# Optimization experiments

Measured on AMD Instinct MI355X. Metric: run time of the kernel, lower is better.

## Reference

```python
import jax, jax.numpy as jnp
import numpy as np

N = 50000
E = 800000
IN_F = 128
HID = 128
OUT_F = 64
MU = 2.0
EPS = 1e-12


def setup_inputs() -> dict:
    key = jax.random.key(0)
    ks = jax.random.split(key, 20)
    d = {}
    d["x"] = jax.random.normal(ks[0], (N, IN_F), dtype=jnp.float32)
    d["edge_src"] = jax.random.randint(ks[1], (E,), 0, N, dtype=jnp.int32)
    d["edge_dst"] = jax.random.randint(ks[2], (E,), 0, N, dtype=jnp.int32)
    d["edge_val"] = jax.random.uniform(ks[3], (E,), dtype=jnp.float32)
    # layer 0: in=128 -> pool=128 -> out=128 (activation=relu)
    s0 = 1.0 / np.sqrt(IN_F)
    d["pool_w0"] = jax.random.uniform(ks[4], (IN_F, IN_F), jnp.float32, -s0, s0)
    d["pool_b0"] = jax.random.uniform(ks[5], (IN_F,), jnp.float32, -s0, s0)
    d["fc1_w0"] = jax.random.uniform(ks[6], (HID, IN_F), jnp.float32, -s0, s0)
    d["fc1_b0"] = jax.random.uniform(ks[7], (HID,), jnp.float32, -s0, s0)
    d["fc2_w0"] = jax.random.uniform(ks[8], (HID, IN_F), jnp.float32, -s0, s0)
    d["fc2_b0"] = jax.random.uniform(ks[9], (HID,), jnp.float32, -s0, s0)
    # layer 1 (final): in=128 -> pool=128 -> out=64 (no activation)
    s1 = 1.0 / np.sqrt(HID)
    d["pool_w1"] = jax.random.uniform(ks[10], (HID, HID), jnp.float32, -s1, s1)
    d["pool_b1"] = jax.random.uniform(ks[11], (HID,), jnp.float32, -s1, s1)
    d["fc1_w1"] = jax.random.uniform(ks[12], (OUT_F, HID), jnp.float32, -s1, s1)
    d["fc1_b1"] = jax.random.uniform(ks[13], (OUT_F,), jnp.float32, -s1, s1)
    d["fc2_w1"] = jax.random.uniform(ks[14], (OUT_F, HID), jnp.float32, -s1, s1)
    d["fc2_b1"] = jax.random.uniform(ks[15], (OUT_F,), jnp.float32, -s1, s1)
    return d


def _sage_conv(x, src, dst, val, pw, pb, w1, b1, w2, b2, act):
    # L2-normalize rows (F.normalize(x, dim=1))
    xn = x / jnp.maximum(jnp.linalg.norm(x, axis=1, keepdims=True), EPS)
    h = jax.nn.relu(xn @ pw.T + pb)               # [N, pool]
    h_mu = h ** MU                                # elementwise pow
    # spmm(adj, h_mu): gather source rows, scale by edge weight, scatter-add to dst rows
    agg = jax.ops.segment_sum(h_mu[src] * val[:, None], dst, num_segments=N)
    agg = agg ** (1.0 / MU)                       # generalized-mean root
    out = (h @ w1.T + b1) + (agg @ w2.T + b2)
    return jax.nn.relu(out) if act else out


def reference(x, edge_src, edge_dst, edge_val,
              pool_w0, pool_b0, fc1_w0, fc1_b0, fc2_w0, fc2_b0,
              pool_w1, pool_b1, fc1_w1, fc1_b1, fc2_w1, fc2_b1):
    h = _sage_conv(x, edge_src, edge_dst, edge_val,
                   pool_w0, pool_b0, fc1_w0, fc1_b0, fc2_w0, fc2_b0, act=True)
    out = _sage_conv(h, edge_src, edge_dst, edge_val,
                     pool_w1, pool_b1, fc1_w1, fc1_b1, fc2_w1, fc2_b1, act=False)
    return out
```

## Files before the change

### kernel.cpp

```cpp
#include <hip/hip_runtime.h>

#define FF 128
#define BCAP 8192
#define CHUNK 4096

typedef __attribute__((ext_vector_type(8))) short short8;
typedef __attribute__((ext_vector_type(4))) float f32x4;

__device__ __forceinline__ unsigned short bf16_rne(float f) {
    unsigned u = __float_as_uint(f);
    u += 0x7fffu + ((u >> 16) & 1u);
    return (unsigned short)(u >> 16);
}
__device__ __forceinline__ float bf16_to_f32(unsigned short h) {
    return __uint_as_float(((unsigned)h) << 16);
}

template<int ABF16>
__global__ __launch_bounds__(256, 2)
void pool_mfma(const void* __restrict__ xin_,
               const unsigned short* __restrict__ Wh, const unsigned short* __restrict__ Wl,
               const float* __restrict__ bias,
               unsigned short* __restrict__ hout, unsigned short* __restrict__ hsqout, int N)
{
    constexpr int PITCH = 136;
    __shared__ unsigned short sX[64 * PITCH];
    __shared__ float sNorm[64];

    const int tid  = threadIdx.x;
    const int tile = blockIdx.x;

    #pragma unroll
    for (int rg = 0; rg < 2; ++rg) {
        const int row = rg * 32 + (tid >> 3);
        const int c0  = (tid & 7) * 16;
        const int n   = tile * 64 + row;
        const int base = row * PITCH + c0;
        float ss = 0.f;
        if constexpr (ABF16) {
            const unsigned short* xin = (const unsigned short*)xin_;
            union { short8 s; unsigned short u[8]; } a, b;
            short8 z = {0,0,0,0,0,0,0,0};
            a.s = z; b.s = z;
            if (n < N) {
                const short8* p = (const short8*)(xin + (size_t)n * FF + c0);
                a.s = p[0]; b.s = p[1];
            }
            #pragma unroll
            for (int i = 0; i < 8; ++i) {
                float fa = bf16_to_f32(a.u[i]);
                float fb = bf16_to_f32(b.u[i]);
                ss = fmaf(fa, fa, fmaf(fb, fb, ss));
            }
            *(short8*)&sX[base]     = a.s;
            *(short8*)&sX[base + 8] = b.s;
        } else {
            const float* xin = (const float*)xin_;
            float v[16];
            if (n < N) {
                const float4* p = (const float4*)(xin + (size_t)n * FF + c0);
                #pragma unroll
                for (int i = 0; i < 4; ++i) {
                    float4 q = p[i];
                    v[4*i] = q.x; v[4*i+1] = q.y; v[4*i+2] = q.z; v[4*i+3] = q.w;
                }
            } else {
                #pragma unroll
                for (int i = 0; i < 16; ++i) v[i] = 0.f;
            }
            #pragma unroll
            for (int i = 0; i < 16; ++i) ss = fmaf(v[i], v[i], ss);
            union { unsigned short u[8]; short8 s; } h0, h1;
            #pragma unroll
            for (int i = 0; i < 8; ++i) {
                h0.u[i] = bf16_rne(v[i]);
                h1.u[i] = bf16_rne(v[8 + i]);
            }
            *(short8*)&sX[base]     = h0.s;
            *(short8*)&sX[base + 8] = h1.s;
        }
        ss += __shfl_xor(ss, 1);
        ss += __shfl_xor(ss, 2);
        ss += __shfl_xor(ss, 4);
        if ((tid & 7) == 0) sNorm[row] = 1.0f / fmaxf(sqrtf(ss), 1e-12f);
    }
    __syncthreads();

    const int lane = tid & 63, wave = tid >> 6;
    const int quad = lane >> 4, l16 = lane & 15;

    short8 Bh[2][4], Bl[2][4];
    #pragma unroll
    for (int c = 0; c < 2; ++c) {
        const int jt = 2 * wave + c;
        #pragma unroll
        for (int t = 0; t < 4; ++t) {
            const size_t o = ((size_t)(jt * 4 + t) * 64 + lane) * 8;
            Bh[c][t] = *(const short8*)&Wh[o];
            Bl[c][t] = *(const short8*)&Wl[o];
        }
    }

    f32x4 acc[4][2];
    #pragma unroll
    for (int r = 0; r < 4; ++r)
        #pragma unroll
        for (int c = 0; c < 2; ++c) {
            f32x4 z = {0.f, 0.f, 0.f, 0.f};
            acc[r][c] = z;
        }

    #pragma unroll
    for (int t = 0; t < 4; ++t) {
        short8 Ah[4];
        #pragma unroll
        for (int r = 0; r < 4; ++r)
            Ah[r] = *(const short8*)&sX[(r * 16 + l16) * PITCH + t * 32 + quad * 8];
        #pragma unroll
        for (int c = 0; c < 2; ++c)
            #pragma unroll
            for (int r = 0; r < 4; ++r) {
                acc[r][c] = __builtin_amdgcn_mfma_f32_16x16x32_bf16(Ah[r], Bh[c][t], acc[r][c], 0, 0, 0);
                acc[r][c] = __builtin_amdgcn_mfma_f32_16x16x32_bf16(Ah[r], Bl[c][t], acc[r][c], 0, 0, 0);
            }
    }

    #pragma unroll
    for (int c = 0; c < 2; ++c) {
        const int j = (2 * wave + c) * 16 + l16;
        const float bj = bias[j];
        #pragma unroll
        for (int r = 0; r < 4; ++r) {
            #pragma unroll
            for (int g = 0; g < 4; ++g) {
                const int nl = r * 16 + quad * 4 + g;
                const int n = tile * 64 + nl;
                if (n < N) {
                    float s = sNorm[nl];
                    float val = fmaf(acc[r][c][g], s, bj);
                    val = fmaxf(val, 0.f);
                    hout  [(size_t)n * FF + j] = bf16_rne(val);
                    hsqout[(size_t)n * FF + j] = bf16_rne(val * val);
                }
            }
        }
    }
}

template<int OUT, int RELU, int OUTBF16>
__global__ __launch_bounds__(256, 2)
void mm2_mfma(const unsigned short* __restrict__ hin,
              const unsigned short* __restrict__ aggh,
              const unsigned short* __restrict__ W1h, const unsigned short* __restrict__ W1l,
              const unsigned short* __restrict__ W2h, const unsigned short* __restrict__ W2l,
              const float* __restrict__ b1, const float* __restrict__ b2,
              void* __restrict__ out_, int N)
{
    constexpr int PITCH = 136;
    __shared__ unsigned short sH [64 * PITCH];
    __shared__ unsigned short sAh[64 * PITCH];

    const int tid  = threadIdx.x;
    const int tile = blockIdx.x;

    #pragma unroll
    for (int rg = 0; rg < 2; ++rg) {
        const int row = rg * 32 + (tid >> 3);
        const int c0  = (tid & 7) * 16;
        const int n   = tile * 64 + row;
        const int base = row * PITCH + c0;
        short8 z = {0,0,0,0,0,0,0,0};
        short8 a = z, b = z, c = z, d = z;
        if (n < N) {
            const short8* ph = (const short8*)(hin  + (size_t)n * FF + c0);
            const short8* pa = (const short8*)(aggh + (size_t)n * FF + c0);
            a = ph[0]; b = ph[1];
            c = pa[0]; d = pa[1];
        }
        *(short8*)&sH [base]     = a;
        *(short8*)&sH [base + 8] = b;
        *(short8*)&sAh[base]     = c;
        *(short8*)&sAh[base + 8] = d;
    }
    __syncthreads();

    const int lane = tid & 63, wave = tid >> 6;
    const int quad = lane >> 4, l16 = lane & 15;
    constexpr int CT = (OUT == 128) ? 2 : 1;

    short8 B1hf[CT][4], B1lf[CT][4], B2hf[CT][4], B2lf[CT][4];
    #pragma unroll
    for (int c = 0; c < CT; ++c) {
        const int jt = (OUT == 128) ? (2 * wave + c) : wave;
        #pragma unroll
        for (int t = 0; t < 4; ++t) {
            const size_t o = ((size_t)(jt * 4 + t) * 64 + lane) * 8;
            B1hf[c][t] = *(const short8*)&W1h[o];
            B1lf[c][t] = *(const short8*)&W1l[o];
            B2hf[c][t] = *(const short8*)&W2h[o];
            B2lf[c][t] = *(const short8*)&W2l[o];
        }
    }

    f32x4 acc[4][CT];
    #pragma unroll
    for (int r = 0; r < 4; ++r)
        #pragma unroll
        for (int c = 0; c < CT; ++c) {
            f32x4 z = {0.f, 0.f, 0.f, 0.f};
            acc[r][c] = z;
        }

    #pragma unroll
    for (int t = 0; t < 4; ++t) {
        short8 Hf[4], AH[4];
        #pragma unroll
        for (int r = 0; r < 4; ++r) {
            const int off = (r * 16 + l16) * PITCH + t * 32 + quad * 8;
            Hf[r] = *(const short8*)&sH[off];
            AH[r] = *(const short8*)&sAh[off];
        }
        #pragma unroll
        for (int c = 0; c < CT; ++c)
            #pragma unroll
            for (int r = 0; r < 4; ++r) {
                acc[r][c] = __builtin_amdgcn_mfma_f32_16x16x32_bf16(Hf[r], B1hf[c][t], acc[r][c], 0, 0, 0);
                acc[r][c] = __builtin_amdgcn_mfma_f32_16x16x32_bf16(Hf[r], B1lf[c][t], acc[r][c], 0, 0, 0);
                acc[r][c] = __builtin_amdgcn_mfma_f32_16x16x32_bf16(AH[r], B2hf[c][t], acc[r][c], 0, 0, 0);
                acc[r][c] = __builtin_amdgcn_mfma_f32_16x16x32_bf16(AH[r], B2lf[c][t], acc[r][c], 0, 0, 0);
            }
    }

    #pragma unroll
    for (int c = 0; c < CT; ++c) {
        const int jt = (OUT == 128) ? (2 * wave + c) : wave;
        const int j = jt * 16 + l16;
        const float bj = b1[j] + b2[j];
        #pragma unroll
        for (int r = 0; r < 4; ++r) {
            #pragma unroll
            for (int g = 0; g < 4; ++g) {
                const int n = tile * 64 + r * 16 + quad * 4 + g;
                if (n < N) {
                    float val = acc[r][c][g] + bj;
                    if constexpr (RELU) val = fmaxf(val, 0.f);
                    if constexpr (OUTBF16)
                        ((unsigned short*)out_)[(size_t)n * OUT + j] = bf16_rne(val);
                    else
                        ((float*)out_)[(size_t)n * OUT + j] = val;
                }
            }
        }
    }
}

struct WPack {
    const float* src[6];
    unsigned short* hi[6];
    unsigned short* lo[6];
    int n[6];
};

__global__ __launch_bounds__(256)
void wprep_kernel(WPack p, int* __restrict__ bucket_cnt)
{
    if (blockIdx.x == 0) bucket_cnt[threadIdx.x] = 0;
    int id = blockIdx.x * 256 + threadIdx.x;
    #pragma unroll
    for (int i = 0; i < 6; ++i) {
        if (id < p.n[i]) {
            float f = p.src[i][id];
            unsigned short h = bf16_rne(f);
            const int j = id >> 7, k = id & 127;
            const int jt = j >> 4, l16 = j & 15;
            const int t = k >> 5, quad = (k >> 3) & 3, j8 = k & 7;
            const size_t o = ((size_t)((jt * 4 + t) * 4 + quad) * 16 + l16) * 8 + j8;
            p.hi[i][o] = h;
            p.lo[i][o] = bf16_rne(f - bf16_to_f32(h));
            return;
        }
        id -= p.n[i];
    }
}

__global__ __launch_bounds__(256)
void partA_kernel(const int* __restrict__ src, const int* __restrict__ dst,
                  const float* __restrict__ val, int* __restrict__ bucket_cnt,
                  int2* __restrict__ ebuf, int E)
{
    __shared__ int cnt[256], sc[256], excl[256], cur[256], gbase[256];
    __shared__ int2 staged[CHUNK];
    const int t = threadIdx.x;
    const int e0 = blockIdx.x * CHUNK;
    const int n  = min(CHUNK, E - e0);

    cnt[t] = 0;
    __syncthreads();
    for (int i = t; i < n; i += 256)
        atomicAdd(&cnt[((unsigned)dst[e0 + i]) >> 8], 1);
    __syncthreads();

    sc[t] = cnt[t];
    __syncthreads();
    #pragma unroll
    for (int off = 1; off < 256; off <<= 1) {
        int v = (t >= off) ? sc[t - off] : 0;
        __syncthreads();
        sc[t] += v;
        __syncthreads();
    }
    excl[t] = sc[t] - cnt[t];
    cur[t]  = excl[t];
    if (cnt[t] > 0) gbase[t] = atomicAdd(&bucket_cnt[t], cnt[t]);
    __syncthreads();

    for (int i = t; i < n; i += 256) {
        int d = dst[e0 + i];
        int s = src[e0 + i];
        float v = val[e0 + i];
        int b = ((unsigned)d) >> 8;
        int slot = atomicAdd(&cur[b], 1);
        staged[slot] = make_int2((s & 0xffff) | (d << 16), __float_as_int(v));
    }
    __syncthreads();

    for (int p = t; p < n; p += 256) {
        int2 ent = staged[p];
        int b = ((unsigned)ent.x) >> 24;
        int gpos = gbase[b] + (p - excl[b]);
        ebuf[(size_t)b * BCAP + gpos] = ent;
    }
}

__global__ __launch_bounds__(256)
void partB_kernel(const int* __restrict__ bucket_cnt, const int2* __restrict__ ebuf,
                  int* __restrict__ offsets, int2* __restrict__ edata,
                  int N, int E, int nbuck)
{
    __shared__ int pre[256], hist[256], sc[256], excl[256], cur[256];
    const int t = threadIdx.x;
    const int b = blockIdx.x;

    pre[t] = (t < nbuck) ? bucket_cnt[t] : 0;
    __syncthreads();
    #pragma unroll
    for (int off = 1; off < 256; off <<= 1) {
        int v = (t >= off) ? pre[t - off] : 0;
        __syncthreads();
        pre[t] += v;
        __syncthreads();
    }
    const int base = (b == 0) ? 0 : pre[b - 1];
    const int cnt  = pre[b] - base;

    hist[t] = 0;
    __syncthreads();
    const int2* ib = ebuf + (size_t)b * BCAP;
    for (int i = t; i < cnt; i += 256)
        atomicAdd(&hist[(((unsigned)ib[i].x) >> 16) & 255], 1);
    __syncthreads();

    sc[t] = hist[t];
    __syncthreads();
    #pragma unroll
    for (int off = 1; off < 256; off <<= 1) {
        int v = (t >= off) ? sc[t - off] : 0;
        __syncthreads();
        sc[t] += v;
        __syncthreads();
    }
    excl[t] = sc[t] - hist[t];
    cur[t]  = excl[t];

    const int node = b * 256 + t;
    if (node <= N) offsets[node] = base + excl[t];
    __syncthreads();

    for (int i = t; i < cnt; i += 256) {
        int2 ent = ib[i];
        int l = (((unsigned)ent.x) >> 16) & 255;
        int pos = base + atomicAdd(&cur[l], 1);
        edata[pos] = make_int2(ent.x & 0xffff, ent.y);
    }
}

__device__ __forceinline__ void fma4(float4& a, float v, uint2 u) {
    a.x = fmaf(v, __uint_as_float(u.x << 16), a.x);
    a.y = fmaf(v, __uint_as_float(u.x & 0xffff0000u), a.y);
    a.z = fmaf(v, __uint_as_float(u.y << 16), a.z);
    a.w = fmaf(v, __uint_as_float(u.y & 0xffff0000u), a.w);
}

__global__ __launch_bounds__(256)
void agg_kernel(const unsigned short* __restrict__ hsq, const int* __restrict__ offsets,
                const int2* __restrict__ edata,
                unsigned short* __restrict__ aggh, int N)
{
    const int w = blockIdx.x * 8 + (threadIdx.x >> 5);
    if (w >= N) return;
    const int l = threadIdx.x & 31;
    const size_t fo = (size_t)(l * 4);
    int e = offsets[w];
    const int end = offsets[w + 1];

    float4 a0 = {0,0,0,0}, a1 = {0,0,0,0}, a2 = {0,0,0,0}, a3 = {0,0,0,0};

    if ((e & 1) && e < end) {
        int2 ed = edata[e];
        uint2 u = *(const uint2*)&hsq[(size_t)ed.x * FF + fo];
        fma4(a0, __int_as_float(ed.y), u);
        ++e;
    }
    for (; e + 3 < end; e += 4) {
        int4 p0 = *(const int4*)&edata[e];
        int4 p1 = *(const int4*)&edata[e + 2];
        uint2 u0 = *(const uint2*)&hsq[(size_t)p0.x * FF + fo];
        uint2 u1 = *(const uint2*)&hsq[(size_t)p0.z * FF + fo];
        uint2 u2 = *(const uint2*)&hsq[(size_t)p1.x * FF + fo];
        uint2 u3 = *(const uint2*)&hsq[(size_t)p1.z * FF + fo];
        fma4(a0, __int_as_float(p0.y), u0);
        fma4(a1, __int_as_float(p0.w), u1);
        fma4(a2, __int_as_float(p1.y), u2);
        fma4(a3, __int_as_float(p1.w), u3);
    }
    if (e + 1 < end) {
        int4 p = *(const int4*)&edata[e];
        uint2 u0 = *(const uint2*)&hsq[(size_t)p.x * FF + fo];
        uint2 u1 = *(const uint2*)&hsq[(size_t)p.z * FF + fo];
        fma4(a0, __int_as_float(p.y), u0);
        fma4(a1, __int_as_float(p.w), u1);
        e += 2;
    }
    if (e < end) {
        int2 ed = edata[e];
        uint2 u = *(const uint2*)&hsq[(size_t)ed.x * FF + fo];
        fma4(a0, __int_as_float(ed.y), u);
    }

    float4 r;
    r.x = sqrtf(a0.x + a1.x + a2.x + a3.x);
    r.y = sqrtf(a0.y + a1.y + a2.y + a3.y);
    r.z = sqrtf(a0.z + a1.z + a2.z + a3.z);
    r.w = sqrtf(a0.w + a1.w + a2.w + a3.w);

    uint2 hv = { (unsigned)bf16_rne(r.x) | ((unsigned)bf16_rne(r.y) << 16),
                 (unsigned)bf16_rne(r.z) | ((unsigned)bf16_rne(r.w) << 16) };
    *(uint2*)&aggh[(size_t)w * FF + fo] = hv;
}

extern "C" void kernel_launch(void* const* d_in, const int* in_sizes, int n_in,
                              void* d_out, int out_size, void* d_ws, size_t ws_size,
                              hipStream_t stream) {
    const float* x    = (const float*)d_in[0];
    const int*   esrc = (const int*)d_in[1];
    const int*   edst = (const int*)d_in[2];
    const float* eval = (const float*)d_in[3];
    const float* pw0  = (const float*)d_in[4];
    const float* pb0  = (const float*)d_in[5];
    const float* f1w0 = (const float*)d_in[6];
    const float* f1b0 = (const float*)d_in[7];
    const float* f2w0 = (const float*)d_in[8];
    const float* f2b0 = (const float*)d_in[9];
    const float* pw1  = (const float*)d_in[10];
    const float* pb1  = (const float*)d_in[11];
    const float* f1w1 = (const float*)d_in[12];
    const float* f1b1 = (const float*)d_in[13];
    const float* f2w1 = (const float*)d_in[14];
    const float* f2b1 = (const float*)d_in[15];
    float* out = (float*)d_out;

    const int N = in_sizes[0] / FF;
    const int E = in_sizes[1];
    const int nbuck = (N + 255) / 256;

    char* ws = (char*)d_ws;
    const size_t planesz = (size_t)N * FF * 2;
    const size_t A = 256;
    size_t off = 0;
    unsigned short* h    = (unsigned short*)(ws + off); off += (planesz + A - 1) / A * A;
    unsigned short* hsq  = (unsigned short*)(ws + off); off += (planesz + A - 1) / A * A;
    unsigned short* aggh = (unsigned short*)(ws + off); off += (planesz + A - 1) / A * A;
    unsigned short* x1   = (unsigned short*)(ws + off); off += (planesz + A - 1) / A * A;
    int* offsets = (int*)(ws + off); off += ((size_t)(N + 1) * 4 + A - 1) / A * A;
    int* bucket_cnt = (int*)(ws + off); off += (size_t)256 * 4;
    int2* ebuf  = (int2*)(ws + off); off += (size_t)nbuck * BCAP * 8;
    int2* edata = (int2*)(ws + off); off += (size_t)E * 8;
    const int wsz[6] = {128 * FF, 128 * FF, 128 * FF, 128 * FF, 64 * FF, 64 * FF};
    unsigned short* whi[6];
    unsigned short* wlo[6];
    for (int i = 0; i < 6; ++i) {
        whi[i] = (unsigned short*)(ws + off); off += (size_t)wsz[i] * 2;
        wlo[i] = (unsigned short*)(ws + off); off += (size_t)wsz[i] * 2;
    }

    WPack pack;
    const float* wsrc[6] = {pw0, f1w0, f2w0, pw1, f1w1, f2w1};
    int wtotal = 0;
    for (int i = 0; i < 6; ++i) {
        pack.src[i] = wsrc[i]; pack.hi[i] = whi[i]; pack.lo[i] = wlo[i]; pack.n[i] = wsz[i];
        wtotal += wsz[i];
    }

    const int ntiles     = (N + 63) / 64;
    const int nodeblocks = (N + 7) / 8;
    dim3 B(256);

    wprep_kernel<<<(wtotal + 255) / 256, B, 0, stream>>>(pack, bucket_cnt);

    partA_kernel<<<(E + CHUNK - 1) / CHUNK, B, 0, stream>>>(esrc, edst, eval, bucket_cnt, ebuf, E);
    partB_kernel<<<nbuck, B, 0, stream>>>(bucket_cnt, ebuf, offsets, edata, N, E, nbuck);

    pool_mfma<0><<<ntiles, B, 0, stream>>>(x, whi[0], wlo[0], pb0, h, hsq, N);
    agg_kernel<<<nodeblocks, B, 0, stream>>>(hsq, offsets, edata, aggh, N);
    mm2_mfma<128, 1, 1><<<ntiles, B, 0, stream>>>(h, aggh, whi[1], wlo[1], whi[2], wlo[2], f1b0, f2b0, x1, N);

    pool_mfma<1><<<ntiles, B, 0, stream>>>(x1, whi[3], wlo[3], pb1, h, hsq, N);
    agg_kernel<<<nodeblocks, B, 0, stream>>>(hsq, offsets, edata, aggh, N);
    mm2_mfma<64, 0, 0><<<ntiles, B, 0, stream>>>(h, aggh, whi[4], wlo[4], whi[5], wlo[5], f1b1, f2b1, out, N);
}
```

Baseline: 248.6 us.

## Fuse GNN pipeline stages into one persistent cooperative kernel with grid syncs

After: 770.5 us. 3.1x slower.

```diff
diff --git a/kernel.cpp b/kernel.cpp
--- a/kernel.cpp
+++ b/kernel.cpp
@@ -1,8 +1,13 @@
 #include <hip/hip_runtime.h>
+#include <hip/hip_cooperative_groups.h>
+
+namespace cg = cooperative_groups;
 
 #define FF 128
 #define BCAP 8192
 #define CHUNK 4096
+#define PITCH 136
+#define SMEM_BYTES 37376
 
 typedef __attribute__((ext_vector_type(8))) short short8;
 typedef __attribute__((ext_vector_type(4))) float f32x4;
@@ -16,19 +21,35 @@
     return __uint_as_float(((unsigned)h) << 16);
 }
 
+struct MegaArgs {
+    const float* x;
+    const int* esrc; const int* edst; const float* eval;
+    const unsigned short* wh0; const unsigned short* wl0;
+    const unsigned short* wh1; const unsigned short* wl1;
+    const unsigned short* wh2; const unsigned short* wl2;
+    const unsigned short* wh3; const unsigned short* wl3;
+    const unsigned short* wh4; const unsigned short* wl4;
+    const unsigned short* wh5; const unsigned short* wl5;
+    const float* pb0; const float* f1b0; const float* f2b0;
+    const float* pb1; const float* f1b1; const float* f2b1;
+    unsigned short* h; unsigned short* hsq; unsigned short* aggh; unsigned short* x1;
+    int* offsets; int* bucket_cnt;
+    int2* ebuf; int2* edata;
+    float* out;
+    int N, E, ntiles, ngroups, nchunks, nbuck;
+};
+
 template<int ABF16>
-__global__ __launch_bounds__(256, 2)
-void pool_mfma(const void* __restrict__ xin_,
+__device__ __forceinline__
+void pool_tile(char* smem_, const void* xin_,
                const unsigned short* __restrict__ Wh, const unsigned short* __restrict__ Wl,
                const float* __restrict__ bias,
-               unsigned short* __restrict__ hout, unsigned short* __restrict__ hsqout, int N)
+               unsigned short* __restrict__ hout, unsigned short* __restrict__ hsqout,
+               int N, int tile)
 {
-    constexpr int PITCH = 136;
-    __shared__ unsigned short sX[64 * PITCH];
-    __shared__ float sNorm[64];
-
-    const int tid  = threadIdx.x;
-    const int tile = blockIdx.x;
+    unsigned short* sX = (unsigned short*)smem_;
+    float* sNorm = (float*)(smem_ + 64 * PITCH * 2);
+    const int tid = threadIdx.x;
 
     #pragma unroll
     for (int rg = 0; rg < 2; ++rg) {
@@ -145,23 +166,21 @@
             }
         }
     }
+    __syncthreads();
 }
 
 template<int OUT, int RELU, int OUTBF16>
-__global__ __launch_bounds__(256, 2)
-void mm2_mfma(const unsigned short* __restrict__ hin,
-              const unsigned short* __restrict__ aggh,
+__device__ __forceinline__
+void mm2_tile(char* smem_,
+              const unsigned short* __restrict__ hin, const unsigned short* __restrict__ aggh,
               const unsigned short* __restrict__ W1h, const unsigned short* __restrict__ W1l,
               const unsigned short* __restrict__ W2h, const unsigned short* __restrict__ W2l,
               const float* __restrict__ b1, const float* __restrict__ b2,
-              void* __restrict__ out_, int N)
+              void* __restrict__ out_, int N, int tile)
 {
-    constexpr int PITCH = 136;
-    __shared__ unsigned short sH [64 * PITCH];
-    __shared__ unsigned short sAh[64 * PITCH];
-
-    const int tid  = threadIdx.x;
-    const int tile = blockIdx.x;
+    unsigned short* sH  = (unsigned short*)smem_;
+    unsigned short* sAh = (unsigned short*)(smem_ + 64 * PITCH * 2);
+    const int tid = threadIdx.x;
 
     #pragma unroll
     for (int rg = 0; rg < 2; ++rg) {
@@ -252,6 +271,222 @@
             }
         }
     }
+    __syncthreads();
+}
+
+__device__ __forceinline__
+void partA_chunk(char* smem_, const MegaArgs& a, int ch)
+{
+    int* cnt   = (int*)smem_;
+    int* sc    = cnt + 256;
+    int* excl  = sc + 256;
+    int* cur   = excl + 256;
+    int* gbase = cur + 256;
+    int2* staged = (int2*)(smem_ + 5 * 256 * 4);
+    const int t = threadIdx.x;
+    const int e0 = ch * CHUNK;
+    const int n  = min(CHUNK, a.E - e0);
+
+    cnt[t] = 0;
+    __syncthreads();
+    for (int i = t; i < n; i += 256)
+        atomicAdd(&cnt[((unsigned)a.edst[e0 + i]) >> 8], 1);
+    __syncthreads();
+
+    sc[t] = cnt[t];
+    __syncthreads();
+    #pragma unroll
+    for (int off = 1; off < 256; off <<= 1) {
+        int v = (t >= off) ? sc[t - off] : 0;
+        __syncthreads();
+        sc[t] += v;
+        __syncthreads();
+    }
+    excl[t] = sc[t] - cnt[t];
+    cur[t]  = excl[t];
+    if (cnt[t] > 0) gbase[t] = atomicAdd(&a.bucket_cnt[t], cnt[t]);
+    __syncthreads();
+
+    for (int i = t; i < n; i += 256) {
+        int d = a.edst[e0 + i];
+        int s = a.esrc[e0 + i];
+        float v = a.eval[e0 + i];
+        int b = ((unsigned)d) >> 8;
+        int slot = atomicAdd(&cur[b], 1);
+        staged[slot] = make_int2((s & 0xffff) | (d << 16), __float_as_int(v));
+    }
+    __syncthreads();
+
+    for (int p = t; p < n; p += 256) {
+        int2 ent = staged[p];
+        int b = ((unsigned)ent.x) >> 24;
+        int gpos = gbase[b] + (p - excl[b]);
+        a.ebuf[(size_t)b * BCAP + gpos] = ent;
+    }
+    __syncthreads();
+}
+
+__device__ __forceinline__
+void partB_bucket(char* smem_, const MegaArgs& a, int b)
+{
+    int* pre  = (int*)smem_;
+    int* hist = pre + 256;
+    int* sc   = hist + 256;
+    int* excl = sc + 256;
+    int* cur  = excl + 256;
+    const int t = threadIdx.x;
+
+    pre[t] = (t < a.nbuck) ? a.bucket_cnt[t] : 0;
+    __syncthreads();
+    #pragma unroll
+    for (int off = 1; off < 256; off <<= 1) {
+        int v = (t >= off) ? pre[t - off] : 0;
+        __syncthreads();
+        pre[t] += v;
+        __syncthreads();
+    }
+    const int base = (b == 0) ? 0 : pre[b - 1];
+    const int cnt  = pre[b] - base;
+
+    hist[t] = 0;
+    __syncthreads();
+    const int2* ib = a.ebuf + (size_t)b * BCAP;
+    for (int i = t; i < cnt; i += 256)
+        atomicAdd(&hist[(((unsigned)ib[i].x) >> 16) & 255], 1);
+    __syncthreads();
+
+    sc[t] = hist[t];
+    __syncthreads();
+    #pragma unroll
+    for (int off = 1; off < 256; off <<= 1) {
+        int v = (t >= off) ? sc[t - off] : 0;
+        __syncthreads();
+        sc[t] += v;
+        __syncthreads();
+    }
+    excl[t] = sc[t] - hist[t];
+    cur[t]  = excl[t];
+
+    const int node = b * 256 + t;
+    if (node <= a.N) a.offsets[node] = base + excl[t];
+    __syncthreads();
+
+    for (int i = t; i < cnt; i += 256) {
+        int2 ent = ib[i];
+        int l = (((unsigned)ent.x) >> 16) & 255;
+        int pos = base + atomicAdd(&cur[l], 1);
+        a.edata[pos] = make_int2(ent.x & 0xffff, ent.y);
+    }
+    __syncthreads();
+}
+
+__device__ __forceinline__ void fma4(float4& a, float v, uint2 u) {
+    a.x = fmaf(v, __uint_as_float(u.x << 16), a.x);
+    a.y = fmaf(v, __uint_as_float(u.x & 0xffff0000u), a.y);
+    a.z = fmaf(v, __uint_as_float(u.y << 16), a.z);
+    a.w = fmaf(v, __uint_as_float(u.y & 0xffff0000u), a.w);
+}
+
+__device__ __forceinline__
+void agg_group(const unsigned short* __restrict__ hsq, const int* __restrict__ offsets,
+               const int2* __restrict__ edata, unsigned short* __restrict__ aggh,
+               int N, int g)
+{
+    const int w = g * 8 + (threadIdx.x >> 5);
+    if (w >= N) return;
+    const int l = threadIdx.x & 31;
+    const size_t fo = (size_t)(l * 4);
+    int e = offsets[w];
+    const int end = offsets[w + 1];
+
+    float4 a0 = {0,0,0,0}, a1 = {0,0,0,0}, a2 = {0,0,0,0}, a3 = {0,0,0,0};
+
+    if ((e & 1) && e < end) {
+        int2 ed = edata[e];
+        uint2 u = *(const uint2*)&hsq[(size_t)ed.x * FF + fo];
+        fma4(a0, __int_as_float(ed.y), u);
+        ++e;
+    }
+    for (; e + 3 < end; e += 4) {
+        int4 p0 = *(const int4*)&edata[e];
+        int4 p1 = *(const int4*)&edata[e + 2];
+        uint2 u0 = *(const uint2*)&hsq[(size_t)p0.x * FF + fo];
+        uint2 u1 = *(const uint2*)&hsq[(size_t)p0.z * FF + fo];
+        uint2 u2 = *(const uint2*)&hsq[(size_t)p1.x * FF + fo];
+        uint2 u3 = *(const uint2*)&hsq[(size_t)p1.z * FF + fo];
+        fma4(a0, __int_as_float(p0.y), u0);
+        fma4(a1, __int_as_float(p0.w), u1);
+        fma4(a2, __int_as_float(p1.y), u2);
+        fma4(a3, __int_as_float(p1.w), u3);
+    }
+    if (e + 1 < end) {
+        int4 p = *(const int4*)&edata[e];
+        uint2 u0 = *(const uint2*)&hsq[(size_t)p.x * FF + fo];
+        uint2 u1 = *(const uint2*)&hsq[(size_t)p.z * FF + fo];
+        fma4(a0, __int_as_float(p.y), u0);
+        fma4(a1, __int_as_float(p.w), u1);
+        e += 2;
+    }
+    if (e < end) {
+        int2 ed = edata[e];
+        uint2 u = *(const uint2*)&hsq[(size_t)ed.x * FF + fo];
+        fma4(a0, __int_as_float(ed.y), u);
+    }
+
+    float4 r;
+    r.x = sqrtf(a0.x + a1.x + a2.x + a3.x);
+    r.y = sqrtf(a0.y + a1.y + a2.y + a3.y);
+    r.z = sqrtf(a0.z + a1.z + a2.z + a3.z);
+    r.w = sqrtf(a0.w + a1.w + a2.w + a3.w);
+
+    uint2 hv = { (unsigned)bf16_rne(r.x) | ((unsigned)bf16_rne(r.y) << 16),
+                 (unsigned)bf16_rne(r.z) | ((unsigned)bf16_rne(r.w) << 16) };
+    *(uint2*)&aggh[(size_t)w * FF + fo] = hv;
+}
+
+__global__ __launch_bounds__(256, 2)
+void mega_kernel(MegaArgs a)
+{
+    cg::grid_group grid = cg::this_grid();
+    __shared__ alignas(16) char smem[SMEM_BYTES];
+
+    const int p1 = a.nchunks + a.ntiles;
+    for (int it = blockIdx.x; it < p1; it += gridDim.x) {
+        if (it < a.nchunks) partA_chunk(smem, a, it);
+        else pool_tile<0>(smem, a.x, a.wh0, a.wl0, a.pb0, a.h, a.hsq, a.N, it - a.nchunks);
+    }
+    __threadfence();
+    grid.sync();
+
+    for (int b = blockIdx.x; b < a.nbuck; b += gridDim.x)
+        partB_bucket(smem, a, b);
+    __threadfence();
+    grid.sync();
+
+    for (int g = blockIdx.x; g < a.ngroups; g += gridDim.x)
+        agg_group(a.hsq, a.offsets, a.edata, a.aggh, a.N, g);
+    __threadfence();
+    grid.sync();
+
+    for (int t = blockIdx.x; t < a.ntiles; t += gridDim.x)
+        mm2_tile<128, 1, 1>(smem, a.h, a.aggh, a.wh1, a.wl1, a.wh2, a.wl2,
+                            a.f1b0, a.f2b0, (void*)a.x1, a.N, t);
+    __threadfence();
+    grid.sync();
+
+    for (int t = blockIdx.x; t < a.ntiles; t += gridDim.x)
+        pool_tile<1>(smem, a.x1, a.wh3, a.wl3, a.pb1, a.h, a.hsq, a.N, t);
+    __threadfence();
+    grid.sync();
+
+    for (int g = blockIdx.x; g < a.ngroups; g += gridDim.x)
+        agg_group(a.hsq, a.offsets, a.edata, a.aggh, a.N, g);
+    __threadfence();
+    grid.sync();
+
+    for (int t = blockIdx.x; t < a.ntiles; t += gridDim.x)
+        mm2_tile<64, 0, 0>(smem, a.h, a.aggh, a.wh4, a.wl4, a.wh5, a.wl5,
+                           a.f1b1, a.f2b1, (void*)a.out, a.N, t);
 }
 
 struct WPack {
@@ -281,171 +516,6 @@
         }
         id -= p.n[i];
     }
-}
-
-__global__ __launch_bounds__(256)
-void partA_kernel(const int* __restrict__ src, const int* __restrict__ dst,
-                  const float* __restrict__ val, int* __restrict__ bucket_cnt,
-                  int2* __restrict__ ebuf, int E)
-{
-    __shared__ int cnt[256], sc[256], excl[256], cur[256], gbase[256];
-    __shared__ int2 staged[CHUNK];
-    const int t = threadIdx.x;
-    const int e0 = blockIdx.x * CHUNK;
-    const int n  = min(CHUNK, E - e0);
-
-    cnt[t] = 0;
-    __syncthreads();
-    for (int i = t; i < n; i += 256)
-        atomicAdd(&cnt[((unsigned)dst[e0 + i]) >> 8], 1);
-    __syncthreads();
-
-    sc[t] = cnt[t];
-    __syncthreads();
-    #pragma unroll
-    for (int off = 1; off < 256; off <<= 1) {
-        int v = (t >= off) ? sc[t - off] : 0;
-        __syncthreads();
-        sc[t] += v;
-        __syncthreads();
-    }
-    excl[t] = sc[t] - cnt[t];
-    cur[t]  = excl[t];
-    if (cnt[t] > 0) gbase[t] = atomicAdd(&bucket_cnt[t], cnt[t]);
-    __syncthreads();
-
-    for (int i = t; i < n; i += 256) {
-        int d = dst[e0 + i];
-        int s = src[e0 + i];
-        float v = val[e0 + i];
-        int b = ((unsigned)d) >> 8;
-        int slot = atomicAdd(&cur[b], 1);
-        staged[slot] = make_int2((s & 0xffff) | (d << 16), __float_as_int(v));
-    }
-    __syncthreads();
-
-    for (int p = t; p < n; p += 256) {
-        int2 ent = staged[p];
-        int b = ((unsigned)ent.x) >> 24;
-        int gpos = gbase[b] + (p - excl[b]);
-        ebuf[(size_t)b * BCAP + gpos] = ent;
-    }
-}
-
-__global__ __launch_bounds__(256)
-void partB_kernel(const int* __restrict__ bucket_cnt, const int2* __restrict__ ebuf,
-                  int* __restrict__ offsets, int2* __restrict__ edata,
-                  int N, int E, int nbuck)
-{
-    __shared__ int pre[256], hist[256], sc[256], excl[256], cur[256];
-    const int t = threadIdx.x;
-    const int b = blockIdx.x;
-
-    pre[t] = (t < nbuck) ? bucket_cnt[t] : 0;
-    __syncthreads();
-    #pragma unroll
-    for (int off = 1; off < 256; off <<= 1) {
-        int v = (t >= off) ? pre[t - off] : 0;
-        __syncthreads();
-        pre[t] += v;
-        __syncthreads();
-    }
-    const int base = (b == 0) ? 0 : pre[b - 1];
-    const int cnt  = pre[b] - base;
-
-    hist[t] = 0;
-    __syncthreads();
-    const int2* ib = ebuf + (size_t)b * BCAP;
-    for (int i = t; i < cnt; i += 256)
-        atomicAdd(&hist[(((unsigned)ib[i].x) >> 16) & 255], 1);
-    __syncthreads();
-
-    sc[t] = hist[t];
-    __syncthreads();
-    #pragma unroll
-    for (int off = 1; off < 256; off <<= 1) {
-        int v = (t >= off) ? sc[t - off] : 0;
-        __syncthreads();
-        sc[t] += v;
-        __syncthreads();
-    }
-    excl[t] = sc[t] - hist[t];
-    cur[t]  = excl[t];
-
-    const int node = b * 256 + t;
-    if (node <= N) offsets[node] = base + excl[t];
-    __syncthreads();
-
-    for (int i = t; i < cnt; i += 256) {
-        int2 ent = ib[i];
-        int l = (((unsigned)ent.x) >> 16) & 255;
-        int pos = base + atomicAdd(&cur[l], 1);
-        edata[pos] = make_int2(ent.x & 0xffff, ent.y);
-    }
-}
-
-__device__ __forceinline__ void fma4(float4& a, float v, uint2 u) {
-    a.x = fmaf(v, __uint_as_float(u.x << 16), a.x);
-    a.y = fmaf(v, __uint_as_float(u.x & 0xffff0000u), a.y);
-    a.z = fmaf(v, __uint_as_float(u.y << 16), a.z);
-    a.w = fmaf(v, __uint_as_float(u.y & 0xffff0000u), a.w);
-}
-
-__global__ __launch_bounds__(256)
-void agg_kernel(const unsigned short* __restrict__ hsq, const int* __restrict__ offsets,
-                const int2* __restrict__ edata,
-                unsigned short* __restrict__ aggh, int N)
-{
-    const int w = blockIdx.x * 8 + (threadIdx.x >> 5);
-    if (w >= N) return;
-    const int l = threadIdx.x & 31;
-    const size_t fo = (size_t)(l * 4);
-    int e = offsets[w];
-    const int end = offsets[w + 1];
-
-    float4 a0 = {0,0,0,0}, a1 = {0,0,0,0}, a2 = {0,0,0,0}, a3 = {0,0,0,0};
-
-    if ((e & 1) && e < end) {
-        int2 ed = edata[e];
-        uint2 u = *(const uint2*)&hsq[(size_t)ed.x * FF + fo];
-        fma4(a0, __int_as_float(ed.y), u);
-        ++e;
-    }
-    for (; e + 3 < end; e += 4) {
-        int4 p0 = *(const int4*)&edata[e];
-        int4 p1 = *(const int4*)&edata[e + 2];
-        uint2 u0 = *(const uint2*)&hsq[(size_t)p0.x * FF + fo];
-        uint2 u1 = *(const uint2*)&hsq[(size_t)p0.z * FF + fo];
-        uint2 u2 = *(const uint2*)&hsq[(size_t)p1.x * FF + fo];
-        uint2 u3 = *(const uint2*)&hsq[(size_t)p1.z * FF + fo];
-        fma4(a0, __int_as_float(p0.y), u0);
-        fma4(a1, __int_as_float(p0.w), u1);
-        fma4(a2, __int_as_float(p1.y), u2);
-        fma4(a3, __int_as_float(p1.w), u3);
-    }
-    if (e + 1 < end) {
-        int4 p = *(const int4*)&edata[e];
-        uint2 u0 = *(const uint2*)&hsq[(size_t)p.x * FF + fo];
-        uint2 u1 = *(const uint2*)&hsq[(size_t)p.z * FF + fo];
-        fma4(a0, __int_as_float(p.y), u0);
-        fma4(a1, __int_as_float(p.w), u1);
-        e += 2;
-    }
-    if (e < end) {
-        int2 ed = edata[e];
-        uint2 u = *(const uint2*)&hsq[(size_t)ed.x * FF + fo];
-        fma4(a0, __int_as_float(ed.y), u);
-    }
-
-    float4 r;
-    r.x = sqrtf(a0.x + a1.x + a2.x + a3.x);
-    r.y = sqrtf(a0.y + a1.y + a2.y + a3.y);
-    r.z = sqrtf(a0.z + a1.z + a2.z + a3.z);
-    r.w = sqrtf(a0.w + a1.w + a2.w + a3.w);
-
-    uint2 hv = { (unsigned)bf16_rne(r.x) | ((unsigned)bf16_rne(r.y) << 16),
-                 (unsigned)bf16_rne(r.z) | ((unsigned)bf16_rne(r.w) << 16) };
-    *(uint2*)&aggh[(size_t)w * FF + fo] = hv;
 }
 
 extern "C" void kernel_launch(void* const* d_in, const int* in_sizes, int n_in,
@@ -501,20 +571,36 @@
         wtotal += wsz[i];
     }
 
-    const int ntiles     = (N + 63) / 64;
-    const int nodeblocks = (N + 7) / 8;
     dim3 B(256);
 
     wprep_kernel<<<(wtotal + 255) / 256, B, 0, stream>>>(pack, bucket_cnt);
 
-    partA_kernel<<<(E + CHUNK - 1) / CHUNK, B, 0, stream>>>(esrc, edst, eval, bucket_cnt, ebuf, E);
-    partB_kernel<<<nbuck, B, 0, stream>>>(bucket_cnt, ebuf, offsets, edata, N, E, nbuck);
-
-    pool_mfma<0><<<ntiles, B, 0, stream>>>(x, whi[0], wlo[0], pb0, h, hsq, N);
-    agg_kernel<<<nodeblocks, B, 0, stream>>>(hsq, offsets, edata, aggh, N);
-    mm2_mfma<128, 1, 1><<<ntiles, B, 0, stream>>>(h, aggh, whi[1], wlo[1], whi[2], wlo[2], f1b0, f2b0, x1, N);
-
-    pool_mfma<1><<<ntiles, B, 0, stream>>>(x1, whi[3], wlo[3], pb1, h, hsq, N);
-    agg_kernel<<<nodeblocks, B, 0, stream>>>(hsq, offsets, edata, aggh, N);
-    mm2_mfma<64, 0, 0><<<ntiles, B, 0, stream>>>(h, aggh, whi[4], wlo[4], whi[5], wlo[5], f1b1, f2b1, out, N);
-}
+    MegaArgs ma;
+    ma.x = x; ma.esrc = esrc; ma.edst = edst; ma.eval = eval;
+    ma.wh0 = whi[0]; ma.wl0 = wlo[0];
+    ma.wh1 = whi[1]; ma.wl1 = wlo[1];
+    ma.wh2 = whi[2]; ma.wl2 = wlo[2];
+    ma.wh3 = whi[3]; ma.wl3 = wlo[3];
+    ma.wh4 = whi[4]; ma.wl4 = wlo[4];
+    ma.wh5 = whi[5]; ma.wl5 = wlo[5];
+    ma.pb0 = pb0; ma.f1b0 = f1b0; ma.f2b0 = f2b0;
+    ma.pb1 = pb1; ma.f1b1 = f1b1; ma.f2b1 = f2b1;
+    ma.h = h; ma.hsq = hsq; ma.aggh = aggh; ma.x1 = x1;
+    ma.offsets = offsets; ma.bucket_cnt = bucket_cnt;
+    ma.ebuf = ebuf; ma.edata = edata;
+    ma.out = out;
+    ma.N = N; ma.E = E;
+    ma.ntiles  = (N + 63) / 64;
+    ma.ngroups = (N + 7) / 8;
+    ma.nchunks = (E + CHUNK - 1) / CHUNK;
+    ma.nbuck   = nbuck;
+
+    int nb = 0;
+    hipOccupancyMaxActiveBlocksPerMultiprocessor(&nb, mega_kernel, 256, 0);
+    if (nb < 1) nb = 1;
+    int grid = nb * 256;
+    if (grid > 2048) grid = 2048;
+
+    void* kargs[] = { (void*)&ma };
+    hipLaunchCooperativeKernel(mega_kernel, dim3(grid), B, kargs, (unsigned)0, stream);
+}
```
